# Optimization experiments

Hardware: AMD Instinct MI355X
Metric: run time of the kernel (lower is better)

## Reference

```python
import jax, jax.numpy as jnp
import numpy as np

B, T, M, C, H = 2, 2048, 2048, 1024, 16
D = C // H  # head_size = 64


def setup_inputs() -> dict:
    key = jax.random.key(0)
    ks = jax.random.split(key, 8)
    s = 0.02
    return {
        "relative_positions": jax.random.normal(ks[0], (H, T, T + M), jnp.float32),
        "x": jax.random.normal(ks[1], (B, T, C), jnp.float32),
        "xl_memory": jax.random.normal(ks[2], (B, M, 2, C), jnp.float32),
        "Wq": jax.random.normal(ks[3], (C, C), jnp.float32) * s,
        "Wk": jax.random.normal(ks[4], (C, C), jnp.float32) * s,
        "Wv": jax.random.normal(ks[5], (C, C), jnp.float32) * s,
        "Wp": jax.random.normal(ks[6], (C, C), jnp.float32) * s,
        "bp": jax.random.normal(ks[7], (C,), jnp.float32) * s,
    }


def reference(relative_positions, x, xl_memory, Wq, Wk, Wv, Wp, bp):
    b, t, c = x.shape
    h, d = H, D
    q = x @ Wq  # [b,t,c]
    k = x @ Wk
    v = x @ Wv
    k_xl = xl_memory[..., 0, :]  # [b,m,c]
    v_xl = xl_memory[..., 1, :]
    k = jnp.concatenate([k_xl, k], axis=-2)  # [b,t+m,c]
    v = jnp.concatenate([v_xl, v], axis=-2)
    tk = k.shape[1]

    def split_heads(z):  # [b,s,(h d)] -> [b,h,s,d]
        return z.reshape(z.shape[0], z.shape[1], h, d).transpose(0, 2, 1, 3)

    qh, kh, vh = split_heads(q), split_heads(k), split_heads(v)
    w = jnp.einsum("bhid,bhjd->bhij", qh, kh)  # [b,h,t,tk]
    i, j = w.shape[-2], w.shape[-1]
    # bias added BEFORE scaling, as in the original
    w = (w + relative_positions[..., -i:, -j:]) * (d ** -0.5)
    # causal mask with memory offset: mask where col > row + (j - i)
    row = jnp.arange(i)[:, None]
    col = jnp.arange(j)[None, :]
    mask = col > row + (j - i)
    w = jnp.where(mask, -jnp.inf, w)
    w = jax.nn.softmax(w, axis=-1)
    wv = jnp.einsum("bhij,bhjd->bhid", w, vh)  # [b,h,t,d]
    wv = wv.transpose(0, 2, 1, 3).reshape(b, t, c)
    out = wv @ Wp + bp
    # rebuild xl memory from full-length k,v, keep last T steps
    k_flat = kh.transpose(0, 2, 1, 3).reshape(b, tk, c)
    v_flat = vh.transpose(0, 2, 1, 3).reshape(b, tk, c)
    new_xl_memory = jnp.stack([k_flat, v_flat], axis=-2)[:, -t:]  # [b,t,2,c]
    return out, new_xl_memory
```

## Files before the change

### kernel.cpp

```cpp
#include <hip/hip_runtime.h>
#include <hip/hip_bf16.h>

constexpr int NB  = 2;
constexpr int TT  = 2048;
constexpr int MEM = 2048;
constexpr int CC  = 1024;
constexpr int NH  = 16;
constexpr int HD  = 64;
constexpr int TKK = 4096;
constexpr int BT  = NB * TT;

typedef __attribute__((ext_vector_type(8))) short short8;
typedef __attribute__((ext_vector_type(4))) float floatx4;

struct __align__(8) us4 { unsigned short x, y, z, w; };

__device__ __forceinline__ unsigned short f2bf(float f) {
  union { float f; unsigned int u; } v; v.f = f;
  return (unsigned short)((v.u + 0x7fffu + ((v.u >> 16) & 1u)) >> 16);
}

__global__ __launch_bounds__(256) void prep_xl_k(const float* __restrict__ xl,
    unsigned short* __restrict__ k_ws, unsigned short* __restrict__ v_ws) {
  int idx = blockIdx.x * 256 + threadIdx.x;
  int c   = (idx & 255) << 2;
  int rem = idx >> 8;
  int m   = rem & 2047;
  int b   = rem >> 11;
  size_t src = ((size_t)(b * MEM + m)) * 2 * CC + c;
  float4 kk = *(const float4*)&xl[src];
  float4 vv = *(const float4*)&xl[src + CC];
  int h = c >> 6, d = c & 63;
  size_t dst = ((size_t)((b * NH + h) * TKK) + m) * HD + d;
  *(us4*)&k_ws[dst] = us4{f2bf(kk.x), f2bf(kk.y), f2bf(kk.z), f2bf(kk.w)};
  *(us4*)&v_ws[dst] = us4{f2bf(vv.x), f2bf(vv.y), f2bf(vv.z), f2bf(vv.w)};
}

__global__ __launch_bounds__(256) void gemm_qkv_k(
    const float* __restrict__ x, const float* __restrict__ Wq,
    const float* __restrict__ Wk, const float* __restrict__ Wv,
    unsigned short* __restrict__ q_ws, unsigned short* __restrict__ k_ws,
    unsigned short* __restrict__ v_ws, float* __restrict__ out_xl) {
  __shared__ unsigned short As[128][32];
  __shared__ unsigned short Bs[128][40];
  const int tid = threadIdx.x;
  const int m0 = blockIdx.x * 128;
  const int nb = blockIdx.y;
  const float* __restrict__ Wsrc = (nb < 8) ? Wq : ((nb < 16) ? Wk : Wv);
  const int n0 = (nb & 7) * 128;
  const int wave = tid >> 6, lane = tid & 63;
  const int mh = (wave >> 1) * 64, nh = (wave & 1) * 64;
  const int ln = lane & 15, qd = lane >> 4;
  const floatx4 fzero = {0.f, 0.f, 0.f, 0.f};

  floatx4 acc[4][4];
#pragma unroll
  for (int i = 0; i < 4; i++)
#pragma unroll
    for (int j = 0; j < 4; j++) acc[i][j] = fzero;

  for (int kt = 0; kt < CC; kt += 32) {
    __syncthreads();
#pragma unroll
    for (int i = 0; i < 4; i++) {
      int e = tid + i * 256;
      int row = e >> 3, kc = (e & 7) << 2;
      float4 a4 = *(const float4*)&x[(size_t)(m0 + row) * CC + kt + kc];
      *(us4*)&As[row][kc] = us4{f2bf(a4.x), f2bf(a4.y), f2bf(a4.z), f2bf(a4.w)};
    }
#pragma unroll
    for (int i = 0; i < 4; i++) {
      int e = tid + i * 256;
      int n = e & 127, kg = e >> 7;
      const float* p = &Wsrc[(size_t)(kt + kg * 4) * CC + n0 + n];
      float b0 = p[0], b1 = p[CC], b2 = p[2 * CC], b3 = p[3 * CC];
      *(us4*)&Bs[n][kg * 4] = us4{f2bf(b0), f2bf(b1), f2bf(b2), f2bf(b3)};
    }
    __syncthreads();
    short8 af[4], bfr[4];
#pragma unroll
    for (int mf = 0; mf < 4; mf++) af[mf]  = *(const short8*)&As[mh + mf * 16 + ln][qd * 8];
#pragma unroll
    for (int nf = 0; nf < 4; nf++) bfr[nf] = *(const short8*)&Bs[nh + nf * 16 + ln][qd * 8];
#pragma unroll
    for (int mf = 0; mf < 4; mf++)
#pragma unroll
      for (int nf = 0; nf < 4; nf++)
        acc[mf][nf] = __builtin_amdgcn_mfma_f32_16x16x32_bf16(af[mf], bfr[nf], acc[mf][nf], 0, 0, 0);
  }

  const int sel = nb >> 3;
#pragma unroll
  for (int mf = 0; mf < 4; mf++) {
#pragma unroll
    for (int nf = 0; nf < 4; nf++) {
      int gn = n0 + nh + nf * 16 + ln;
      int h = gn >> 6, d = gn & 63;
#pragma unroll
      for (int r = 0; r < 4; r++) {
        int gm = m0 + mh + mf * 16 + qd * 4 + r;
        int b = gm >> 11, t = gm & 2047;
        float val = acc[mf][nf][r];
        unsigned short bv = f2bf(val);
        if (sel == 0) {
          q_ws[((size_t)((b * NH + h) * TT) + t) * HD + d] = bv;
        } else if (sel == 1) {
          k_ws[((size_t)((b * NH + h) * TKK) + MEM + t) * HD + d] = bv;
          out_xl[(((size_t)(b * TT + t)) * 2 + 0) * CC + gn] = val;
        } else {
          v_ws[((size_t)((b * NH + h) * TKK) + MEM + t) * HD + d] = bv;
          out_xl[(((size_t)(b * TT + t)) * 2 + 1) * CC + gn] = val;
        }
      }
    }
  }
}

__global__ __launch_bounds__(256) void attn_k(
    const unsigned short* __restrict__ q_ws, const unsigned short* __restrict__ k_ws,
    const unsigned short* __restrict__ v_ws, const float* __restrict__ rel,
    unsigned short* __restrict__ wv_ws) {
  __shared__ unsigned short Ks[NB][64][72];
  __shared__ unsigned short Vs[NB][64][64];
  __shared__ unsigned short Ps[4][16][64];
  const int qt = blockIdx.x, h = blockIdx.y;
  const int tid = threadIdx.x;
  const int wave = tid >> 6, lane = tid & 63;
  const int ln = lane & 15, qd = lane >> 4;
  const int q0 = qt * 64;
  const int qrow_w = q0 + wave * 16;
  const floatx4 fzero = {0.f, 0.f, 0.f, 0.f};

  short8 qf[NB][2];
#pragma unroll
  for (int b = 0; b < NB; b++)
#pragma unroll
    for (int ks = 0; ks < 2; ks++)
      qf[b][ks] = *(const short8*)&q_ws[((size_t)((b * NH + h) * TT) + qrow_w + ln) * HD + ks * 32 + qd * 8];

  floatx4 of[NB][4];
  float mrow[NB][4], lrow[NB][4];
#pragma unroll
  for (int b = 0; b < NB; b++) {
#pragma unroll
    for (int nf = 0; nf < 4; nf++) of[b][nf] = fzero;
#pragma unroll
    for (int r = 0; r < 4; r++) { mrow[b][r] = -1e30f; lrow[b][r] = 0.f; }
  }

  const int ntiles = qt + 33;
  for (int kt = 0; kt < ntiles; kt++) {
    const int kbase = kt * 64;
    __syncthreads();
#pragma unroll
    for (int b = 0; b < NB; b++) {
      const size_t rowbase = (size_t)((b * NH + h) * TKK) + kbase;
#pragma unroll
      for (int i = 0; i < 2; i++) {
        int e = tid + i * 256;
        int r = e >> 3, c0 = (e & 7) << 3;
        *(short8*)&Ks[b][r][c0] = *(const short8*)&k_ws[(rowbase + r) * HD + c0];
        short8 v8 = *(const short8*)&v_ws[(rowbase + r) * HD + c0];
#pragma unroll
        for (int j = 0; j < 8; j++) {
          int d = c0 + j;
          int slot = ((r >> 3) ^ (d & 7) ^ (d >> 3)) & 7;
          Vs[b][d][(slot << 3) | (r & 7)] = (unsigned short)v8[j];
        }
      }
    }
    __syncthreads();

    float bias[4][4];
#pragma unroll
    for (int nf = 0; nf < 4; nf++)
#pragma unroll
      for (int r = 0; r < 4; r++)
        bias[nf][r] = rel[((size_t)(h * TT) + qrow_w + qd * 4 + r) * TKK + kbase + nf * 16 + ln];

    const bool lastTile = (kt == ntiles - 1);

#pragma unroll
    for (int b = 0; b < NB; b++) {
      floatx4 sacc[4];
#pragma unroll
      for (int nf = 0; nf < 4; nf++) sacc[nf] = fzero;
#pragma unroll
      for (int ks = 0; ks < 2; ks++)
#pragma unroll
        for (int nf = 0; nf < 4; nf++) {
          short8 kf = *(const short8*)&Ks[b][nf * 16 + ln][ks * 32 + qd * 8];
          sacc[nf] = __builtin_amdgcn_mfma_f32_16x16x32_bf16(qf[b][ks], kf, sacc[nf], 0, 0, 0);
        }

      float sv[4][4];
#pragma unroll
      for (int nf = 0; nf < 4; nf++)
#pragma unroll
        for (int r = 0; r < 4; r++)
          sv[nf][r] = (sacc[nf][r] + bias[nf][r]) * 0.125f;
      if (lastTile) {
#pragma unroll
        for (int nf = 0; nf < 4; nf++)
#pragma unroll
          for (int r = 0; r < 4; r++) {
            int kcol = kbase + nf * 16 + ln;
            int qrow = qrow_w + qd * 4 + r;
            if (kcol > qrow + MEM) sv[nf][r] = -1e30f;
          }
      }

#pragma unroll
      for (int r = 0; r < 4; r++) {
        float mx = fmaxf(fmaxf(sv[0][r], sv[1][r]), fmaxf(sv[2][r], sv[3][r]));
#pragma unroll
        for (int off = 8; off >= 1; off >>= 1)
          mx = fmaxf(mx, __shfl_xor(mx, off, 64));
        float mnew = fmaxf(mrow[b][r], mx);
        float alpha = __expf(mrow[b][r] - mnew);
        mrow[b][r] = mnew;
        float sum = 0.f;
#pragma unroll
        for (int nf = 0; nf < 4; nf++) {
          float p = __expf(sv[nf][r] - mnew);
          sv[nf][r] = p;
          sum += p;
        }
#pragma unroll
        for (int off = 8; off >= 1; off >>= 1)
          sum += __shfl_xor(sum, off, 64);
        lrow[b][r] = lrow[b][r] * alpha + sum;
#pragma unroll
        for (int nf = 0; nf < 4; nf++) of[b][nf][r] *= alpha;
      }

#pragma unroll
      for (int nf = 0; nf < 4; nf++)
#pragma unroll
        for (int r = 0; r < 4; r++) {
          int row = qd * 4 + r;
          int col = nf * 16 + ln;
          int slot = ((col >> 3) ^ (row & 7) ^ (row >> 3)) & 7;
          Ps[wave][row][(slot << 3) | (col & 7)] = f2bf(sv[nf][r]);
        }

#pragma unroll
      for (int ks = 0; ks < 2; ks++) {
        int g = qd + 4 * ks;
        int pslot = (g ^ (ln & 7) ^ (ln >> 3)) & 7;
        short8 pf = *(const short8*)&Ps[wave][ln][pslot << 3];
#pragma unroll
        for (int nf = 0; nf < 4; nf++) {
          int dd = nf * 16 + ln;
          int vslot = (g ^ (dd & 7) ^ (dd >> 3)) & 7;
          short8 vf = *(const short8*)&Vs[b][dd][vslot << 3];
          of[b][nf] = __builtin_amdgcn_mfma_f32_16x16x32_bf16(pf, vf, of[b][nf], 0, 0, 0);
        }
      }
    }
  }

#pragma unroll
  for (int b = 0; b < NB; b++) {
    float inv[4];
#pragma unroll
    for (int r = 0; r < 4; r++) inv[r] = 1.f / lrow[b][r];
#pragma unroll
    for (int nf = 0; nf < 4; nf++)
#pragma unroll
      for (int r = 0; r < 4; r++)
        wv_ws[((size_t)(b * TT) + qrow_w + qd * 4 + r) * CC + h * 64 + nf * 16 + ln] =
            f2bf(of[b][nf][r] * inv[r]);
  }
}

__global__ __launch_bounds__(256) void gemm_out_k(
    const unsigned short* __restrict__ a_bf, const float* __restrict__ Wp,
    const float* __restrict__ bp, float* __restrict__ out) {
  __shared__ unsigned short As[128][32];
  __shared__ unsigned short Bs[128][40];
  const int tid = threadIdx.x;
  const int m0 = blockIdx.x * 128;
  const int n0 = blockIdx.y * 128;
  const int wave = tid >> 6, lane = tid & 63;
  const int mh = (wave >> 1) * 64, nh = (wave & 1) * 64;
  const int ln = lane & 15, qd = lane >> 4;
  const floatx4 fzero = {0.f, 0.f, 0.f, 0.f};

  floatx4 acc[4][4];
#pragma unroll
  for (int i = 0; i < 4; i++)
#pragma unroll
    for (int j = 0; j < 4; j++) acc[i][j] = fzero;

  for (int kt = 0; kt < CC; kt += 32) {
    __syncthreads();
#pragma unroll
    for (int i = 0; i < 2; i++) {
      int e = tid + i * 256;
      int row = e >> 2, c0 = (e & 3) << 3;
      *(short8*)&As[row][c0] = *(const short8*)&a_bf[(size_t)(m0 + row) * CC + kt + c0];
    }
#pragma unroll
    for (int i = 0; i < 4; i++) {
      int e = tid + i * 256;
      int n = e & 127, kg = e >> 7;
      const float* p = &Wp[(size_t)(kt + kg * 4) * CC + n0 + n];
      float b0 = p[0], b1 = p[CC], b2 = p[2 * CC], b3 = p[3 * CC];
      *(us4*)&Bs[n][kg * 4] = us4{f2bf(b0), f2bf(b1), f2bf(b2), f2bf(b3)};
    }
    __syncthreads();
    short8 af[4], bfr[4];
#pragma unroll
    for (int mf = 0; mf < 4; mf++) af[mf]  = *(const short8*)&As[mh + mf * 16 + ln][qd * 8];
#pragma unroll
    for (int nf = 0; nf < 4; nf++) bfr[nf] = *(const short8*)&Bs[nh + nf * 16 + ln][qd * 8];
#pragma unroll
    for (int mf = 0; mf < 4; mf++)
#pragma unroll
      for (int nf = 0; nf < 4; nf++)
        acc[mf][nf] = __builtin_amdgcn_mfma_f32_16x16x32_bf16(af[mf], bfr[nf], acc[mf][nf], 0, 0, 0);
  }

#pragma unroll
  for (int mf = 0; mf < 4; mf++)
#pragma unroll
    for (int nf = 0; nf < 4; nf++) {
      int gn = n0 + nh + nf * 16 + ln;
      float bias = bp[gn];
#pragma unroll
      for (int r = 0; r < 4; r++) {
        int gm = m0 + mh + mf * 16 + qd * 4 + r;
        out[(size_t)gm * CC + gn] = acc[mf][nf][r] + bias;
      }
    }
}

extern "C" void kernel_launch(void* const* d_in, const int* in_sizes, int n_in,
                              void* d_out, int out_size, void* d_ws, size_t ws_size,
                              hipStream_t stream) {
  const float* rel = (const float*)d_in[0];
  const float* x   = (const float*)d_in[1];
  const float* xl  = (const float*)d_in[2];
  const float* Wq  = (const float*)d_in[3];
  const float* Wk  = (const float*)d_in[4];
  const float* Wv  = (const float*)d_in[5];
  const float* Wp  = (const float*)d_in[6];
  const float* bp  = (const float*)d_in[7];
  float* out    = (float*)d_out;
  float* out_xl = out + (size_t)BT * CC;

  char* ws = (char*)d_ws;
  unsigned short* q_ws  = (unsigned short*)(ws);
  unsigned short* k_ws  = (unsigned short*)(ws + (size_t)(8)  * 1024 * 1024);
  unsigned short* v_ws  = (unsigned short*)(ws + (size_t)(24) * 1024 * 1024);
  unsigned short* wv_ws = (unsigned short*)(ws + (size_t)(40) * 1024 * 1024);

  prep_xl_k<<<dim3(4096), dim3(256), 0, stream>>>(xl, k_ws, v_ws);
  gemm_qkv_k<<<dim3(32, 24), dim3(256), 0, stream>>>(x, Wq, Wk, Wv, q_ws, k_ws, v_ws, out_xl);
  attn_k<<<dim3(32, 16), dim3(256), 0, stream>>>(q_ws, k_ws, v_ws, rel, wv_ws);
  gemm_out_k<<<dim3(32, 8), dim3(256), 0, stream>>>(wv_ws, Wp, bp, out);
}
```

Before: 1.047 ms.

## Split attention blocks per batch and schedule heaviest query tiles first

The attention kernel now launches one block per (batch, head, query tile) instead of processing both batches in one block. Blocks are ordered with the longest causal rows first and with adjacent blocks sharing the same head and tile, so the relative-position bias can be reused through cache. This halves per-block registers and shared memory, raising occupancy and improving load balance. The risk is that the bias tensor is read twice unless the two batch blocks hit in L2.

```diff
diff --git a/kernel.cpp b/kernel.cpp
--- a/kernel.cpp
+++ b/kernel.cpp
@@ -120,10 +120,13 @@
     const unsigned short* __restrict__ q_ws, const unsigned short* __restrict__ k_ws,
     const unsigned short* __restrict__ v_ws, const float* __restrict__ rel,
     unsigned short* __restrict__ wv_ws) {
-  __shared__ unsigned short Ks[NB][64][72];
-  __shared__ unsigned short Vs[NB][64][64];
+  __shared__ unsigned short Ks[64][72];
+  __shared__ unsigned short Vs[64][64];
   __shared__ unsigned short Ps[4][16][64];
-  const int qt = blockIdx.x, h = blockIdx.y;
+  const int idx = blockIdx.x;
+  const int qt = 31 - (idx >> 5);
+  const int h  = (idx >> 1) & 15;
+  const int b  = idx & 1;
   const int tid = threadIdx.x;
   const int wave = tid >> 6, lane = tid & 63;
   const int ln = lane & 15, qd = lane >> 4;
@@ -131,41 +134,35 @@
   const int qrow_w = q0 + wave * 16;
   const floatx4 fzero = {0.f, 0.f, 0.f, 0.f};
 
-  short8 qf[NB][2];
-#pragma unroll
-  for (int b = 0; b < NB; b++)
-#pragma unroll
-    for (int ks = 0; ks < 2; ks++)
-      qf[b][ks] = *(const short8*)&q_ws[((size_t)((b * NH + h) * TT) + qrow_w + ln) * HD + ks * 32 + qd * 8];
-
-  floatx4 of[NB][4];
-  float mrow[NB][4], lrow[NB][4];
-#pragma unroll
-  for (int b = 0; b < NB; b++) {
-#pragma unroll
-    for (int nf = 0; nf < 4; nf++) of[b][nf] = fzero;
-#pragma unroll
-    for (int r = 0; r < 4; r++) { mrow[b][r] = -1e30f; lrow[b][r] = 0.f; }
-  }
+  short8 qf[2];
+#pragma unroll
+  for (int ks = 0; ks < 2; ks++)
+    qf[ks] = *(const short8*)&q_ws[((size_t)((b * NH + h) * TT) + qrow_w + ln) * HD + ks * 32 + qd * 8];
+
+  floatx4 of[4];
+  float mrow[4], lrow[4];
+#pragma unroll
+  for (int nf = 0; nf < 4; nf++) of[nf] = fzero;
+#pragma unroll
+  for (int r = 0; r < 4; r++) { mrow[r] = -1e30f; lrow[r] = 0.f; }
 
   const int ntiles = qt + 33;
   for (int kt = 0; kt < ntiles; kt++) {
     const int kbase = kt * 64;
     __syncthreads();
-#pragma unroll
-    for (int b = 0; b < NB; b++) {
+    {
       const size_t rowbase = (size_t)((b * NH + h) * TKK) + kbase;
 #pragma unroll
       for (int i = 0; i < 2; i++) {
         int e = tid + i * 256;
         int r = e >> 3, c0 = (e & 7) << 3;
-        *(short8*)&Ks[b][r][c0] = *(const short8*)&k_ws[(rowbase + r) * HD + c0];
+        *(short8*)&Ks[r][c0] = *(const short8*)&k_ws[(rowbase + r) * HD + c0];
         short8 v8 = *(const short8*)&v_ws[(rowbase + r) * HD + c0];
 #pragma unroll
         for (int j = 0; j < 8; j++) {
           int d = c0 + j;
           int slot = ((r >> 3) ^ (d & 7) ^ (d >> 3)) & 7;
-          Vs[b][d][(slot << 3) | (r & 7)] = (unsigned short)v8[j];
+          Vs[d][(slot << 3) | (r & 7)] = (unsigned short)v8[j];
         }
       }
     }
@@ -180,97 +177,93 @@
 
     const bool lastTile = (kt == ntiles - 1);
 
-#pragma unroll
-    for (int b = 0; b < NB; b++) {
-      floatx4 sacc[4];
-#pragma unroll
-      for (int nf = 0; nf < 4; nf++) sacc[nf] = fzero;
-#pragma unroll
-      for (int ks = 0; ks < 2; ks++)
-#pragma unroll
-        for (int nf = 0; nf < 4; nf++) {
-          short8 kf = *(const short8*)&Ks[b][nf * 16 + ln][ks * 32 + qd * 8];
-          sacc[nf] = __builtin_amdgcn_mfma_f32_16x16x32_bf16(qf[b][ks], kf, sacc[nf], 0, 0, 0);
+    floatx4 sacc[4];
+#pragma unroll
+    for (int nf = 0; nf < 4; nf++) sacc[nf] = fzero;
+#pragma unroll
+    for (int ks = 0; ks < 2; ks++)
+#pragma unroll
+      for (int nf = 0; nf < 4; nf++) {
+        short8 kf = *(const short8*)&Ks[nf * 16 + ln][ks * 32 + qd * 8];
+        sacc[nf] = __builtin_amdgcn_mfma_f32_16x16x32_bf16(qf[ks], kf, sacc[nf], 0, 0, 0);
+      }
+
+    float sv[4][4];
+#pragma unroll
+    for (int nf = 0; nf < 4; nf++)
+#pragma unroll
+      for (int r = 0; r < 4; r++)
+        sv[nf][r] = (sacc[nf][r] + bias[nf][r]) * 0.125f;
+    if (lastTile) {
+#pragma unroll
+      for (int nf = 0; nf < 4; nf++)
+#pragma unroll
+        for (int r = 0; r < 4; r++) {
+          int kcol = kbase + nf * 16 + ln;
+          int qrow = qrow_w + qd * 4 + r;
+          if (kcol > qrow + MEM) sv[nf][r] = -1e30f;
         }
-
-      float sv[4][4];
-#pragma unroll
-      for (int nf = 0; nf < 4; nf++)
-#pragma unroll
-        for (int r = 0; r < 4; r++)
-          sv[nf][r] = (sacc[nf][r] + bias[nf][r]) * 0.125f;
-      if (lastTile) {
-#pragma unroll
-        for (int nf = 0; nf < 4; nf++)
-#pragma unroll
-          for (int r = 0; r < 4; r++) {
-            int kcol = kbase + nf * 16 + ln;
-            int qrow = qrow_w + qd * 4 + r;
-            if (kcol > qrow + MEM) sv[nf][r] = -1e30f;
-          }
-      }
-
+    }
+
+#pragma unroll
+    for (int r = 0; r < 4; r++) {
+      float mx = fmaxf(fmaxf(sv[0][r], sv[1][r]), fmaxf(sv[2][r], sv[3][r]));
+#pragma unroll
+      for (int off = 8; off >= 1; off >>= 1)
+        mx = fmaxf(mx, __shfl_xor(mx, off, 64));
+      float mnew = fmaxf(mrow[r], mx);
+      float alpha = __expf(mrow[r] - mnew);
+      mrow[r] = mnew;
+      float sum = 0.f;
+#pragma unroll
+      for (int nf = 0; nf < 4; nf++) {
+        float p = __expf(sv[nf][r] - mnew);
+        sv[nf][r] = p;
+        sum += p;
+      }
+#pragma unroll
+      for (int off = 8; off >= 1; off >>= 1)
+        sum += __shfl_xor(sum, off, 64);
+      lrow[r] = lrow[r] * alpha + sum;
+#pragma unroll
+      for (int nf = 0; nf < 4; nf++) of[nf][r] *= alpha;
+    }
+
+#pragma unroll
+    for (int nf = 0; nf < 4; nf++)
 #pragma unroll
       for (int r = 0; r < 4; r++) {
-        float mx = fmaxf(fmaxf(sv[0][r], sv[1][r]), fmaxf(sv[2][r], sv[3][r]));
-#pragma unroll
-        for (int off = 8; off >= 1; off >>= 1)
-          mx = fmaxf(mx, __shfl_xor(mx, off, 64));
-        float mnew = fmaxf(mrow[b][r], mx);
-        float alpha = __expf(mrow[b][r] - mnew);
-        mrow[b][r] = mnew;
-        float sum = 0.f;
-#pragma unroll
-        for (int nf = 0; nf < 4; nf++) {
-          float p = __expf(sv[nf][r] - mnew);
-          sv[nf][r] = p;
-          sum += p;
-        }
-#pragma unroll
-        for (int off = 8; off >= 1; off >>= 1)
-          sum += __shfl_xor(sum, off, 64);
-        lrow[b][r] = lrow[b][r] * alpha + sum;
-#pragma unroll
-        for (int nf = 0; nf < 4; nf++) of[b][nf][r] *= alpha;
-      }
-
-#pragma unroll
-      for (int nf = 0; nf < 4; nf++)
-#pragma unroll
-        for (int r = 0; r < 4; r++) {
-          int row = qd * 4 + r;
-          int col = nf * 16 + ln;
-          int slot = ((col >> 3) ^ (row & 7) ^ (row >> 3)) & 7;
-          Ps[wave][row][(slot << 3) | (col & 7)] = f2bf(sv[nf][r]);
-        }
-
-#pragma unroll
-      for (int ks = 0; ks < 2; ks++) {
-        int g = qd + 4 * ks;
-        int pslot = (g ^ (ln & 7) ^ (ln >> 3)) & 7;
-        short8 pf = *(const short8*)&Ps[wave][ln][pslot << 3];
-#pragma unroll
-        for (int nf = 0; nf < 4; nf++) {
-          int dd = nf * 16 + ln;
-          int vslot = (g ^ (dd & 7) ^ (dd >> 3)) & 7;
-          short8 vf = *(const short8*)&Vs[b][dd][vslot << 3];
-          of[b][nf] = __builtin_amdgcn_mfma_f32_16x16x32_bf16(pf, vf, of[b][nf], 0, 0, 0);
-        }
-      }
-    }
-  }
-
-#pragma unroll
-  for (int b = 0; b < NB; b++) {
+        int row = qd * 4 + r;
+        int col = nf * 16 + ln;
+        int slot = ((col >> 3) ^ (row & 7) ^ (row >> 3)) & 7;
+        Ps[wave][row][(slot << 3) | (col & 7)] = f2bf(sv[nf][r]);
+      }
+
+#pragma unroll
+    for (int ks = 0; ks < 2; ks++) {
+      int g = qd + 4 * ks;
+      int pslot = (g ^ (ln & 7) ^ (ln >> 3)) & 7;
+      short8 pf = *(const short8*)&Ps[wave][ln][pslot << 3];
+#pragma unroll
+      for (int nf = 0; nf < 4; nf++) {
+        int dd = nf * 16 + ln;
+        int vslot = (g ^ (dd & 7) ^ (dd >> 3)) & 7;
+        short8 vf = *(const short8*)&Vs[dd][vslot << 3];
+        of[nf] = __builtin_amdgcn_mfma_f32_16x16x32_bf16(pf, vf, of[nf], 0, 0, 0);
+      }
+    }
+  }
+
+  {
     float inv[4];
 #pragma unroll
-    for (int r = 0; r < 4; r++) inv[r] = 1.f / lrow[b][r];
+    for (int r = 0; r < 4; r++) inv[r] = 1.f / lrow[r];
 #pragma unroll
     for (int nf = 0; nf < 4; nf++)
 #pragma unroll
       for (int r = 0; r < 4; r++)
         wv_ws[((size_t)(b * TT) + qrow_w + qd * 4 + r) * CC + h * 64 + nf * 16 + ln] =
-            f2bf(of[b][nf][r] * inv[r]);
+            f2bf(of[nf][r] * inv[r]);
   }
 }
 
@@ -358,6 +351,6 @@
 
   prep_xl_k<<<dim3(4096), dim3(256), 0, stream>>>(xl, k_ws, v_ws);
   gemm_qkv_k<<<dim3(32, 24), dim3(256), 0, stream>>>(x, Wq, Wk, Wv, q_ws, k_ws, v_ws, out_xl);
-  attn_k<<<dim3(32, 16), dim3(256), 0, stream>>>(q_ws, k_ws, v_ws, rel, wv_ws);
+  attn_k<<<dim3(1024), dim3(256), 0, stream>>>(q_ws, k_ws, v_ws, rel, wv_ws);
   gemm_out_k<<<dim3(32, 8), dim3(256), 0, stream>>>(wv_ws, Wp, bp, out);
 }
```

Result: faster. 1.002 ms (-4.3%).
